# Performance work log

Measured on AMD Instinct MI355X. Metric: run time of the kernel, lower is better.

## Reference

```python
import jax, jax.numpy as jnp
import numpy as np

B, S, D = 2, 2048, 1024
H, DQK, DV = 16, 64, 64

def setup_inputs() -> dict:
    key = jax.random.key(0)
    k1, k2, k3, k4, k5 = jax.random.split(key, 5)
    scale_in = 1.0 / np.sqrt(D)
    scale_v = 1.0 / np.sqrt(H * DV)
    return {
        "x":   jax.random.normal(k1, (B, S, D), dtype=jnp.float32),
        "W_q": jax.random.uniform(k2, (D, H * DQK), minval=-scale_in, maxval=scale_in, dtype=jnp.float32),
        "W_k": jax.random.uniform(k3, (D, H * DQK), minval=-scale_in, maxval=scale_in, dtype=jnp.float32),
        "W_v": jax.random.uniform(k4, (D, H * DV), minval=-scale_in, maxval=scale_in, dtype=jnp.float32),
        "W_o": jax.random.uniform(k5, (H * DV, D), minval=-scale_v, maxval=scale_v, dtype=jnp.float32),
    }

def reference(x, W_q, W_k, W_v, W_o):
    b, s, _ = x.shape
    # projections -> [B, H, S, d]
    Q = (x @ W_q).reshape(b, s, H, DQK).transpose(0, 2, 1, 3)
    K = (x @ W_k).reshape(b, s, H, DQK).transpose(0, 2, 1, 3)
    V = (x @ W_v).reshape(b, s, H, DV).transpose(0, 2, 1, 3)
    scores = jnp.einsum('bhqd,bhkd->bhqk', Q, K) / np.sqrt(DQK).astype(np.float32)
    causal_mask = jnp.triu(jnp.ones((s, s), dtype=bool), k=1)  # True above diagonal
    scores = jnp.where(causal_mask[None, None], -jnp.inf, scores)
    attn = jax.nn.softmax(scores, axis=-1)
    out = jnp.einsum('bhqk,bhkd->bhqd', attn, V)  # [B,H,S,DV]
    out = out.transpose(0, 2, 1, 3).reshape(b, s, H * DV)
    return out @ W_o
```

## Files before the change

kernel.cpp:

```cpp
#include <hip/hip_runtime.h>


typedef float  f32x4  __attribute__((ext_vector_type(4)));
typedef __bf16 bf16x8 __attribute__((ext_vector_type(8)));

__device__ __forceinline__ unsigned short f2bf(float f) {
    __bf16 h = (__bf16)f;
    return __builtin_bit_cast(unsigned short, h);
}

__device__ __forceinline__ void gld16(unsigned short* lds, const unsigned short* g) {
    __builtin_amdgcn_global_load_lds(
        (const __attribute__((address_space(1))) void*)g,
        (__attribute__((address_space(3))) void*)lds, 16, 0, 0);
}

__global__ __launch_bounds__(256) void prep(const float* __restrict__ x,
                                            const float* __restrict__ W0,
                                            const float* __restrict__ W1,
                                            const float* __restrict__ W2,
                                            const float* __restrict__ W3,
                                            unsigned short* __restrict__ xb,
                                            unsigned short* __restrict__ WT) {
    __shared__ float T[64][65];
    const int blk = blockIdx.x;
    const int tid = threadIdx.x;
    if (blk < 4096) {
        size_t i = ((size_t)blk * 256 + tid) * 4;
        float4 v = *(const float4*)(x + i);
        ushort4 o;
        o.x = f2bf(v.x); o.y = f2bf(v.y); o.z = f2bf(v.z); o.w = f2bf(v.w);
        *(ushort4*)(xb + i) = o;
        return;
    }
    const int t = blk - 4096;
    const int z = t >> 8;
    const int k0 = ((t >> 4) & 15) * 64, n0 = (t & 15) * 64;
    const float* W = (z == 0) ? W0 : (z == 1) ? W1 : (z == 2) ? W2 : W3;
#pragma unroll
    for (int i = 0; i < 4; i++) {
        int c = tid + i * 256;
        int r = c >> 4, col = (c & 15) * 4;
        float4 v = *(const float4*)(W + (size_t)(k0 + r) * 1024 + n0 + col);
        T[r][col] = v.x; T[r][col + 1] = v.y; T[r][col + 2] = v.z; T[r][col + 3] = v.w;
    }
    __syncthreads();
    unsigned short* out = WT + (size_t)z * 1024 * 1024;
#pragma unroll
    for (int i = 0; i < 2; i++) {
        int c = tid + i * 256;
        int nr = c >> 3, koff = (c & 7) * 8;
        union { unsigned short us[8]; uint4 v; } pk;
#pragma unroll
        for (int j = 0; j < 8; j++) pk.us[j] = f2bf(T[koff + j][nr]);
        *(uint4*)(out + (size_t)(n0 + nr) * 1024 + k0 + koff) = pk.v;
    }
}

__global__ __launch_bounds__(256) void gemm_qkv(const unsigned short* __restrict__ A,
                                                const unsigned short* __restrict__ WTall,
                                                unsigned short* __restrict__ outq,
                                                unsigned short* __restrict__ Vp) {
    __shared__ unsigned short As0[128 * 64];
    __shared__ unsigned short Bs0[128 * 64];
    __shared__ unsigned short As1[128 * 64];
    __shared__ unsigned short Bs1[128 * 64];
    const int tid = threadIdx.x;
    const int w = tid >> 6, lane = tid & 63, quad = lane >> 4, ln = lane & 15;

    const int blk = blockIdx.x;
    const int n0 = ((blk >> 3) & 7) * 128;
    const int g  = ((blk >> 6) << 3) | (blk & 7);
    const int z  = g >> 5;
    const int m0 = (g & 31) * 128;

    const unsigned short* BT = WTall + (size_t)z * (1024 * 1024);
    const float scl = (z == 0) ? 0.180336878f : 1.0f;
    const bool swp = (z < 2);

    const int lr8 = lane >> 3;
    const int lc8 = ((lane & 7) ^ lr8) * 8;
    const int fsw = (quad ^ (ln & 7)) * 8;

    const f32x4 z4 = {0.f, 0.f, 0.f, 0.f};
    f32x4 acc[4][4];
#pragma unroll
    for (int i = 0; i < 4; i++)
#pragma unroll
        for (int j = 0; j < 4; j++) acc[i][j] = z4;

    const int wm = (w & 1) * 64, wn = (w >> 1) * 64;
    const int Rb = w * 32;

#define QKV_STAGE(Ad, Bd, kk)                                                              \
    {                                                                                      \
        _Pragma("unroll")                                                                  \
        for (int s = 0; s < 4; s++) {                                                      \
            gld16(Ad + (Rb + s * 8) * 64, A  + (size_t)(m0 + Rb + s * 8 + lr8) * 1024 + (kk) + lc8); \
            gld16(Bd + (Rb + s * 8) * 64, BT + (size_t)(n0 + Rb + s * 8 + lr8) * 1024 + (kk) + lc8); \
        }                                                                                  \
    }

#define QKV_COMPUTE(Ad, Bd)                                                                \
    {                                                                                      \
        _Pragma("unroll")                                                                  \
        for (int ks = 0; ks < 2; ks++) {                                                   \
            const int co = fsw ^ (ks * 32);                                                \
            bf16x8 af[4], bfr[4];                                                          \
            _Pragma("unroll")                                                              \
            for (int t = 0; t < 4; t++)                                                    \
                af[t] = *(const bf16x8*)&Ad[(wm + t * 16 + ln) * 64 + co];                 \
            _Pragma("unroll")                                                              \
            for (int t = 0; t < 4; t++)                                                    \
                bfr[t] = *(const bf16x8*)&Bd[(wn + t * 16 + ln) * 64 + co];                \
            if (swp) {                                                                     \
                _Pragma("unroll")                                                          \
                for (int tm = 0; tm < 4; tm++)                                             \
                    _Pragma("unroll")                                                      \
                    for (int tn = 0; tn < 4; tn++)                                         \
                        acc[tm][tn] = __builtin_amdgcn_mfma_f32_16x16x32_bf16(             \
                            bfr[tn], af[tm], acc[tm][tn], 0, 0, 0);                        \
            } else {                                                                       \
                _Pragma("unroll")                                                          \
                for (int tm = 0; tm < 4; tm++)                                             \
                    _Pragma("unroll")                                                      \
                    for (int tn = 0; tn < 4; tn++)                                         \
                        acc[tm][tn] = __builtin_amdgcn_mfma_f32_16x16x32_bf16(             \
                            af[tm], bfr[tn], acc[tm][tn], 0, 0, 0);                        \
            }                                                                              \
        }                                                                                  \
    }

    QKV_STAGE(As0, Bs0, 0);
    for (int k0 = 0; k0 < 1024; k0 += 128) {
        __syncthreads();
        if (k0 + 64 < 1024) QKV_STAGE(As1, Bs1, k0 + 64);
        QKV_COMPUTE(As0, Bs0);
        __syncthreads();
        if (k0 + 128 < 1024) QKV_STAGE(As0, Bs0, k0 + 128);
        if (k0 + 64 < 1024) QKV_COMPUTE(As1, Bs1);
    }
#undef QKV_STAGE
#undef QKV_COMPUTE

    if (swp) {
#pragma unroll
        for (int tm = 0; tm < 4; tm++)
#pragma unroll
            for (int tn = 0; tn < 4; tn++) {
                int mg = m0 + wm + tm * 16 + ln;
                int nb = n0 + wn + tn * 16 + quad * 4;
                int b = mg >> 11, s = mg & 2047, h = nb >> 6, dd = nb & 63;
                ushort4 o;
                o.x = f2bf(acc[tm][tn][0] * scl);
                o.y = f2bf(acc[tm][tn][1] * scl);
                o.z = f2bf(acc[tm][tn][2] * scl);
                o.w = f2bf(acc[tm][tn][3] * scl);
                size_t zoff = (size_t)z * (4096 * 1024);
                *(ushort4*)(outq + zoff + (((size_t)(b * 16 + h) * 2048 + s) << 6) + dd) = o;
            }
    } else {
#pragma unroll
        for (int tm = 0; tm < 4; tm++)
#pragma unroll
            for (int tn = 0; tn < 4; tn++) {
                int mg = m0 + wm + tm * 16 + quad * 4;
                int ng = n0 + wn + tn * 16 + ln;
                int b = mg >> 11, h = ng >> 6, dd = ng & 63;
                int sblk = (mg & 2047) & ~63;
                int cb = tm >> 1, t16 = tm & 1;
                int pp = cb * 32 + quad * 8 + t16 * 4;
                ushort4 o;
                o.x = f2bf(acc[tm][tn][0]);
                o.y = f2bf(acc[tm][tn][1]);
                o.z = f2bf(acc[tm][tn][2]);
                o.w = f2bf(acc[tm][tn][3]);
                *(ushort4*)(Vp + ((size_t)(b * 16 + h) * 64 + dd) * 2048 + sblk + pp) = o;
            }
    }
}

__global__ __launch_bounds__(256) void gemm_o(const unsigned short* __restrict__ A,
                                              const unsigned short* __restrict__ BT,
                                              float* __restrict__ outf) {
    __shared__ unsigned short As0[128 * 64];
    __shared__ unsigned short Bs0[128 * 64];
    __shared__ unsigned short As1[128 * 64];
    __shared__ unsigned short Bs1[128 * 64];
    const int tid = threadIdx.x;
    const int w = tid >> 6, lane = tid & 63, quad = lane >> 4, ln = lane & 15;

    const int blk = blockIdx.x;
    const int n0 = ((blk >> 3) & 7) * 128;
    const int m0 = (((blk >> 6) << 3) | (blk & 7)) * 128;

    const int lr8 = lane >> 3;
    const int lc8 = ((lane & 7) ^ lr8) * 8;
    const int fsw = (quad ^ (ln & 7)) * 8;

    const f32x4 z4 = {0.f, 0.f, 0.f, 0.f};
    f32x4 acc[4][4];
#pragma unroll
    for (int i = 0; i < 4; i++)
#pragma unroll
        for (int j = 0; j < 4; j++) acc[i][j] = z4;

    const int wm = (w & 1) * 64, wn = (w >> 1) * 64;
    const int Rb = w * 32;

#define O_STAGE(Ad, Bd, kk)                                                                \
    {                                                                                      \
        _Pragma("unroll")                                                                  \
        for (int s = 0; s < 4; s++) {                                                      \
            gld16(Ad + (Rb + s * 8) * 64, A  + (size_t)(m0 + Rb + s * 8 + lr8) * 1024 + (kk) + lc8); \
            gld16(Bd + (Rb + s * 8) * 64, BT + (size_t)(n0 + Rb + s * 8 + lr8) * 1024 + (kk) + lc8); \
        }                                                                                  \
    }

#define O_COMPUTE(Ad, Bd)                                                                  \
    {                                                                                      \
        _Pragma("unroll")                                                                  \
        for (int ks = 0; ks < 2; ks++) {                                                   \
            const int co = fsw ^ (ks * 32);                                                \
            bf16x8 af[4], bfr[4];                                                          \
            _Pragma("unroll")                                                              \
            for (int t = 0; t < 4; t++)                                                    \
                af[t] = *(const bf16x8*)&Ad[(wm + t * 16 + ln) * 64 + co];                 \
            _Pragma("unroll")                                                              \
            for (int t = 0; t < 4; t++)                                                    \
                bfr[t] = *(const bf16x8*)&Bd[(wn + t * 16 + ln) * 64 + co];                \
            _Pragma("unroll")                                                              \
            for (int tm = 0; tm < 4; tm++)                                                 \
                _Pragma("unroll")                                                          \
                for (int tn = 0; tn < 4; tn++)                                             \
                    acc[tm][tn] = __builtin_amdgcn_mfma_f32_16x16x32_bf16(                 \
                        bfr[tn], af[tm], acc[tm][tn], 0, 0, 0);                            \
        }                                                                                  \
    }

    O_STAGE(As0, Bs0, 0);
    for (int k0 = 0; k0 < 1024; k0 += 128) {
        __syncthreads();
        if (k0 + 64 < 1024) O_STAGE(As1, Bs1, k0 + 64);
        O_COMPUTE(As0, Bs0);
        __syncthreads();
        if (k0 + 128 < 1024) O_STAGE(As0, Bs0, k0 + 128);
        if (k0 + 64 < 1024) O_COMPUTE(As1, Bs1);
    }
#undef O_STAGE
#undef O_COMPUTE

#pragma unroll
    for (int tm = 0; tm < 4; tm++)
#pragma unroll
        for (int tn = 0; tn < 4; tn++) {
            int mg = m0 + wm + tm * 16 + ln;
            int nb = n0 + wn + tn * 16 + quad * 4;
            *(f32x4*)(outf + (size_t)mg * 1024 + nb) = acc[tm][tn];
        }
}

__global__ __launch_bounds__(512, 4) void flash(const unsigned short* __restrict__ Qb,
                                                const unsigned short* __restrict__ Kb,
                                                const unsigned short* __restrict__ Vpb,
                                                unsigned short* __restrict__ AO,
                                                float* __restrict__ Ph0,
                                                float* __restrict__ Ph1,
                                                float* __restrict__ Lb) {
    __shared__ __align__(16) unsigned short Ks0[64 * 64];
    __shared__ __align__(16) unsigned short Vs0[64 * 64];
    __shared__ __align__(16) unsigned short Ks1[64 * 64];
    __shared__ __align__(16) unsigned short Vs1[64 * 64];
    __shared__ __align__(16) unsigned short Ks2[64 * 64];
    __shared__ __align__(16) unsigned short Vs2[64 * 64];
    const int tid = threadIdx.x, w = tid >> 6, lane = tid & 63;
    const int qd = lane >> 4, ln = lane & 15;
    const int lr = lane >> 3;
    const int lchunk = (lane & 7) ^ lr;
    const int psw = (qd ^ (ln & 7)) * 8;

    const int blk = blockIdx.x;
    const int bh = blk & 31;
    const int s  = blk >> 5;
    int qi, kstart, kend, half;
    bool heavy;
    if (s < 8) {
        qi = s; kstart = 0; kend = (qi + 1) * 128; half = 0; heavy = false;
    } else {
        int t = s - 8; half = t >> 3; qi = 15 - (t & 7); heavy = true;
        int mid = (qi + 1) * 64;
        kstart = half ? mid : 0;
        kend   = half ? (qi + 1) * 128 : mid;
    }
    const int qt0 = qi * 128;

    const unsigned short* Kg = Kb  + (size_t)bh * 2048 * 64;
    const unsigned short* Vg = Vpb + (size_t)bh * 64 * 2048;

    bf16x8 aq[2];
    {
        const unsigned short* Qrow = Qb + ((size_t)bh * 2048 + qt0 + w * 16 + ln) * 64 + qd * 8;
        aq[0] = *(const bf16x8*)(Qrow);
        aq[1] = *(const bf16x8*)(Qrow + 32);
    }

    const f32x4 z4 = {0.f, 0.f, 0.f, 0.f};
    f32x4 Oc[4];
#pragma unroll
    for (int td = 0; td < 4; td++) Oc[td] = z4;
    float lsum = 0.f;

    const int qrow = qt0 + w * 16 + ln;
    const int qmin = qt0 + w * 16;
    const int qmax = qmin + 15;

#define FLASH_STAGE(KD, VD, kk)                                                          \
    {                                                                                    \
        const unsigned short* kg = Kg + (size_t)((kk) + w * 8 + lr) * 64 + lchunk * 8;   \
        gld16(&KD[(w * 8) * 64], kg);                                                    \
        const unsigned short* vg = Vg + (size_t)(w * 8 + lr) * 2048 + (kk) + lchunk * 8; \
        gld16(&VD[(w * 8) * 64], vg);                                                    \
    }

#define FLASH_SYNC(more)                                                                 \
    {                                                                                    \
        if (more) { asm volatile("s_waitcnt vmcnt(2)" ::: "memory"); }                   \
        else      { asm volatile("s_waitcnt vmcnt(0)" ::: "memory"); }                   \
        __builtin_amdgcn_s_barrier();                                                    \
        __builtin_amdgcn_sched_barrier(0);                                               \
    }

#define FLASH_TILE(KD, VD, kk)                                                           \
    if ((kk) <= qmax) {                                                                  \
        f32x4 sc[4];                                                                     \
        _Pragma("unroll")                                                                \
        for (int t = 0; t < 4; t++) {                                                    \
            sc[t] = z4;                                                                  \
            if ((kk) + t * 16 <= qmax) {                                                 \
                int off = (t * 16 + ln) * 64 + psw;                                      \
                bf16x8 bk0 = *(const bf16x8*)&KD[off];                                   \
                bf16x8 bk1 = *(const bf16x8*)&KD[off ^ 32];                              \
                sc[t] = __builtin_amdgcn_mfma_f32_16x16x32_bf16(bk0, aq[0], sc[t], 0, 0, 0); \
                sc[t] = __builtin_amdgcn_mfma_f32_16x16x32_bf16(bk1, aq[1], sc[t], 0, 0, 0); \
            }                                                                            \
        }                                                                                \
        unsigned int pk[4][2];                                                           \
        _Pragma("unroll")                                                                \
        for (int t = 0; t < 4; t++) {                                                    \
            if ((kk) + t * 16 > qmax) { pk[t][0] = 0u; pk[t][1] = 0u; continue; }        \
            float e[4];                                                                  \
            _Pragma("unroll")                                                            \
            for (int r2 = 0; r2 < 4; r2++) e[r2] = __builtin_amdgcn_exp2f(sc[t][r2]);    \
            if ((kk) + t * 16 + 15 > qmin) {                                             \
                _Pragma("unroll")                                                        \
                for (int r2 = 0; r2 < 4; r2++)                                           \
                    if ((kk) + t * 16 + qd * 4 + r2 > qrow) e[r2] = 0.f;                 \
            }                                                                            \
            lsum += (e[0] + e[1]) + (e[2] + e[3]);                                       \
            pk[t][0] = (unsigned int)f2bf(e[0]) | ((unsigned int)f2bf(e[1]) << 16);      \
            pk[t][1] = (unsigned int)f2bf(e[2]) | ((unsigned int)f2bf(e[3]) << 16);      \
        }                                                                                \
        union { unsigned int u[4]; bf16x8 v; } apu0, apu1;                               \
        apu0.u[0] = pk[0][0]; apu0.u[1] = pk[0][1]; apu0.u[2] = pk[1][0]; apu0.u[3] = pk[1][1]; \
        apu1.u[0] = pk[2][0]; apu1.u[1] = pk[2][1]; apu1.u[2] = pk[3][0]; apu1.u[3] = pk[3][1]; \
        _Pragma("unroll")                                                                \
        for (int td = 0; td < 4; td++) {                                                 \
            int voff = (td * 16 + ln) * 64 + psw;                                        \
            bf16x8 av0 = *(const bf16x8*)&VD[voff];                                      \
            bf16x8 av1 = *(const bf16x8*)&VD[voff ^ 32];                                 \
            Oc[td] = __builtin_amdgcn_mfma_f32_16x16x32_bf16(av0, apu0.v, Oc[td], 0, 0, 0); \
            Oc[td] = __builtin_amdgcn_mfma_f32_16x16x32_bf16(av1, apu1.v, Oc[td], 0, 0, 0); \
        }                                                                                \
    }

    FLASH_STAGE(Ks0, Vs0, kstart);
    if (kstart + 64 < kend) FLASH_STAGE(Ks1, Vs1, kstart + 64);

    for (int k0 = kstart; k0 < kend; k0 += 192) {
        FLASH_SYNC(k0 + 64 < kend);
        if (k0 + 128 < kend) FLASH_STAGE(Ks2, Vs2, k0 + 128);
        FLASH_TILE(Ks0, Vs0, k0);
        if (k0 + 64 < kend) {
            FLASH_SYNC(k0 + 128 < kend);
            if (k0 + 192 < kend) FLASH_STAGE(Ks0, Vs0, k0 + 192);
            FLASH_TILE(Ks1, Vs1, k0 + 64);
        }
        if (k0 + 128 < kend) {
            FLASH_SYNC(k0 + 192 < kend);
            if (k0 + 256 < kend) FLASH_STAGE(Ks1, Vs1, k0 + 256);
            FLASH_TILE(Ks2, Vs2, k0 + 128);
        }
    }
#undef FLASH_STAGE
#undef FLASH_SYNC
#undef FLASH_TILE

    lsum += __shfl_xor(lsum, 16);
    lsum += __shfl_xor(lsum, 32);

    if (!heavy) {
        const float inv = 1.0f / lsum;
        const int bz = bh >> 4, h = bh & 15;
        const int rowg = qt0 + w * 16 + ln;
        unsigned short* aorow = AO + ((size_t)(bz * 2048 + rowg) << 10) + h * 64 + qd * 4;
#pragma unroll
        for (int td = 0; td < 4; td++) {
            ushort4 o;
            o.x = f2bf(Oc[td][0] * inv);
            o.y = f2bf(Oc[td][1] * inv);
            o.z = f2bf(Oc[td][2] * inv);
            o.w = f2bf(Oc[td][3] * inv);
            *(ushort4*)(aorow + td * 16) = o;
        }
    } else {
        float* P = half ? Ph1 : Ph0;
        const int prow = ((bh * 8 + (qi - 8)) * 128) + w * 16 + ln;
        float* Pr = P + (size_t)prow * 64 + qd * 4;
#pragma unroll
        for (int td = 0; td < 4; td++)
            *(f32x4*)(Pr + td * 16) = Oc[td];
        if (qd == 0) Lb[half * 32768 + prow] = lsum;
    }
}

__global__ __launch_bounds__(256) void merge(const float* __restrict__ P0,
                                             const float* __restrict__ P1,
                                             const float* __restrict__ Lb,
                                             unsigned short* __restrict__ AO) {
    const int idx = blockIdx.x * 256 + threadIdx.x;
    const int d0 = (idx & 7) * 8;
    const int row = idx >> 3;
    const float inv = 1.0f / (Lb[row] + Lb[32768 + row]);
    const float* a = P0 + (size_t)row * 64 + d0;
    const float* b = P1 + (size_t)row * 64 + d0;
    f32x4 x0 = *(const f32x4*)a, x1 = *(const f32x4*)(a + 4);
    f32x4 y0 = *(const f32x4*)b, y1 = *(const f32x4*)(b + 4);
    union { unsigned short us[8]; uint4 v; } pk;
#pragma unroll
    for (int j = 0; j < 4; j++) {
        pk.us[j]     = f2bf((x0[j] + y0[j]) * inv);
        pk.us[j + 4] = f2bf((x1[j] + y1[j]) * inv);
    }
    const int bh = row >> 10, qi8 = (row >> 7) & 7, q = row & 127;
    const int bz = bh >> 4, h = bh & 15;
    const int rowg = (qi8 + 8) * 128 + q;
    *(uint4*)(AO + ((size_t)(bz * 2048 + rowg) << 10) + h * 64 + d0) = pk.v;
}

extern "C" void kernel_launch(void* const* d_in, const int* in_sizes, int n_in,
                              void* d_out, int out_size, void* d_ws, size_t ws_size,
                              hipStream_t stream) {
    const float* x  = (const float*)d_in[0];
    const float* Wq = (const float*)d_in[1];
    const float* Wk = (const float*)d_in[2];
    const float* Wv = (const float*)d_in[3];
    const float* Wo = (const float*)d_in[4];
    float* out = (float*)d_out;

    unsigned short* xb  = (unsigned short*)d_ws;
    unsigned short* WT  = xb  + (size_t)4096 * 1024;
    unsigned short* Qb  = WT  + (size_t)4 * 1024 * 1024;
    unsigned short* Kb  = Qb  + (size_t)4096 * 1024;
    unsigned short* Vb  = Kb  + (size_t)4096 * 1024;
    unsigned short* Vpb = Vb  + (size_t)4096 * 1024;
    unsigned short* AO  = Vpb + (size_t)4096 * 1024;

    float* Ph0 = (float*)Vb;
    float* Ph1 = (float*)xb;
    float* Lb  = (float*)WT;

    prep<<<dim3(5120), 256, 0, stream>>>(x, Wq, Wk, Wv, Wo, xb, WT);
    gemm_qkv<<<dim3(768), 256, 0, stream>>>(xb, WT, Qb, Vpb);
    flash<<<dim3(768), 512, 0, stream>>>(Qb, Kb, Vpb, AO, Ph0, Ph1, Lb);
    merge<<<dim3(1024), 256, 0, stream>>>(Ph0, Ph1, Lb, AO);
    gemm_o<<<dim3(256), 256, 0, stream>>>(AO, WT + (size_t)3 * 1024 * 1024, out);
}
```

Measured before the change: 166.8 us.

## Fuse split-K merge into flash kernel via last-block atomic counter

Removes the separate merge kernel launch. Each heavy query tile is split across two blocks, and those blocks now increment an atomic counter that lives in an AO slot zeroed by prep. Whichever block arrives second combines the two partial outputs and their normalizers and writes bf16 to AO. This saves one kernel launch and its dependency gap, at the cost of a threadfence, two extra barriers in the heavy blocks, and a serial tail in the finishing block. The counter slot is overwritten later with real output by the merging block.

```diff
diff --git a/kernel.cpp b/kernel.cpp
--- a/kernel.cpp
+++ b/kernel.cpp
@@ -21,7 +21,8 @@
                                             const float* __restrict__ W2,
                                             const float* __restrict__ W3,
                                             unsigned short* __restrict__ xb,
-                                            unsigned short* __restrict__ WT) {
+                                            unsigned short* __restrict__ WT,
+                                            unsigned short* __restrict__ AO) {
     __shared__ float T[64][65];
     const int blk = blockIdx.x;
     const int tid = threadIdx.x;
@@ -31,6 +32,11 @@
         ushort4 o;
         o.x = f2bf(v.x); o.y = f2bf(v.y); o.z = f2bf(v.z); o.w = f2bf(v.w);
         *(ushort4*)(xb + i) = o;
+        if (blk == 0) {
+            const int bh = tid >> 3, qi8 = tid & 7;
+            const int bz = bh >> 4, h = bh & 15;
+            *(unsigned int*)(AO + (((size_t)(bz * 2048 + (qi8 + 8) * 128)) << 10) + h * 64) = 0u;
+        }
         return;
     }
     const int t = blk - 4096;
@@ -273,6 +279,7 @@
     __shared__ __align__(16) unsigned short Vs1[64 * 64];
     __shared__ __align__(16) unsigned short Ks2[64 * 64];
     __shared__ __align__(16) unsigned short Vs2[64 * 64];
+    __shared__ unsigned int s_last;
     const int tid = threadIdx.x, w = tid >> 6, lane = tid & 63;
     const int qd = lane >> 4, ln = lane & 15;
     const int lr = lane >> 3;
@@ -414,37 +421,46 @@
         }
     } else {
         float* P = half ? Ph1 : Ph0;
-        const int prow = ((bh * 8 + (qi - 8)) * 128) + w * 16 + ln;
+        const int pidx = bh * 8 + (qi - 8);
+        const int prow = pidx * 128 + w * 16 + ln;
         float* Pr = P + (size_t)prow * 64 + qd * 4;
 #pragma unroll
         for (int td = 0; td < 4; td++)
             *(f32x4*)(Pr + td * 16) = Oc[td];
         if (qd == 0) Lb[half * 32768 + prow] = lsum;
-    }
-}
-
-__global__ __launch_bounds__(256) void merge(const float* __restrict__ P0,
-                                             const float* __restrict__ P1,
-                                             const float* __restrict__ Lb,
-                                             unsigned short* __restrict__ AO) {
-    const int idx = blockIdx.x * 256 + threadIdx.x;
-    const int d0 = (idx & 7) * 8;
-    const int row = idx >> 3;
-    const float inv = 1.0f / (Lb[row] + Lb[32768 + row]);
-    const float* a = P0 + (size_t)row * 64 + d0;
-    const float* b = P1 + (size_t)row * 64 + d0;
-    f32x4 x0 = *(const f32x4*)a, x1 = *(const f32x4*)(a + 4);
-    f32x4 y0 = *(const f32x4*)b, y1 = *(const f32x4*)(b + 4);
-    union { unsigned short us[8]; uint4 v; } pk;
-#pragma unroll
-    for (int j = 0; j < 4; j++) {
-        pk.us[j]     = f2bf((x0[j] + y0[j]) * inv);
-        pk.us[j + 4] = f2bf((x1[j] + y1[j]) * inv);
-    }
-    const int bh = row >> 10, qi8 = (row >> 7) & 7, q = row & 127;
-    const int bz = bh >> 4, h = bh & 15;
-    const int rowg = (qi8 + 8) * 128 + q;
-    *(uint4*)(AO + ((size_t)(bz * 2048 + rowg) << 10) + h * 64 + d0) = pk.v;
+
+        const int bz = bh >> 4, h = bh & 15;
+        __threadfence();
+        __syncthreads();
+        if (tid == 0) {
+            unsigned int* flagp = (unsigned int*)(AO +
+                (((size_t)(bz * 2048 + qt0)) << 10) + h * 64);
+            s_last = atomicAdd(flagp, 1u);
+        }
+        __syncthreads();
+        if (s_last == 1u) {
+            __threadfence();
+            const int rbase = pidx * 128;
+#pragma unroll
+            for (int i = 0; i < 2; i++) {
+                int c = tid + i * 512;
+                int q = c >> 3, d0 = (c & 7) * 8;
+                int r = rbase + q;
+                float invl = 1.0f / (Lb[r] + Lb[32768 + r]);
+                const float* a = Ph0 + (size_t)r * 64 + d0;
+                const float* b = Ph1 + (size_t)r * 64 + d0;
+                f32x4 x0 = *(const f32x4*)a, x1 = *(const f32x4*)(a + 4);
+                f32x4 y0 = *(const f32x4*)b, y1 = *(const f32x4*)(b + 4);
+                union { unsigned short us[8]; uint4 v; } pkk;
+#pragma unroll
+                for (int j = 0; j < 4; j++) {
+                    pkk.us[j]     = f2bf((x0[j] + y0[j]) * invl);
+                    pkk.us[j + 4] = f2bf((x1[j] + y1[j]) * invl);
+                }
+                *(uint4*)(AO + (((size_t)(bz * 2048 + qt0 + q)) << 10) + h * 64 + d0) = pkk.v;
+            }
+        }
+    }
 }
 
 extern "C" void kernel_launch(void* const* d_in, const int* in_sizes, int n_in,
@@ -469,9 +485,8 @@
     float* Ph1 = (float*)xb;
     float* Lb  = (float*)WT;
 
-    prep<<<dim3(5120), 256, 0, stream>>>(x, Wq, Wk, Wv, Wo, xb, WT);
+    prep<<<dim3(5120), 256, 0, stream>>>(x, Wq, Wk, Wv, Wo, xb, WT, AO);
     gemm_qkv<<<dim3(768), 256, 0, stream>>>(xb, WT, Qb, Vpb);
     flash<<<dim3(768), 512, 0, stream>>>(Qb, Kb, Vpb, AO, Ph0, Ph1, Lb);
-    merge<<<dim3(1024), 256, 0, stream>>>(Ph0, Ph1, Lb, AO);
     gemm_o<<<dim3(256), 256, 0, stream>>>(AO, WT + (size_t)3 * 1024 * 1024, out);
 }
```

After: 310.7 us. 1.86x slower.
